# Optimization experiments

Measured on AMD Instinct MI355X. Metric: run time of the kernel, lower is better.

Reference implementation:

```python
import jax, jax.numpy as jnp
import numpy as np

ALPHA = 0.05      # SSGConv alpha
K_HOPS = 2        # SSGConv K
K_EIG = 16        # Laplacian PE eigenvectors
LN_EPS = 1e-5     # nn.LayerNorm default eps


def setup_inputs() -> dict:
    key = jax.random.key(0)
    ks = jax.random.split(key, 8)
    B, N, T, D = 16, 19, 1024, 64
    return {
        "features": jax.random.normal(ks[0], (B, N, T, D), jnp.float32),
        "adjacency": jax.random.uniform(ks[1], (B, T, N, N), jnp.float32),
        # edge_transform: nn.Linear(1,1)
        "edge_w": jax.random.normal(ks[2], (), jnp.float32) * 0.5,
        "edge_b": jnp.zeros((), jnp.float32),
        # SSGConv internal linear layers (out = h @ W.T + b)
        "gnn0_W": jax.random.normal(ks[3], (D, D + K_EIG), jnp.float32) / jnp.sqrt(jnp.float32(D + K_EIG)),
        "gnn0_b": jnp.zeros((D,), jnp.float32),
        "gnn1_W": jax.random.normal(ks[4], (D, D), jnp.float32) / jnp.sqrt(jnp.float32(D)),
        "gnn1_b": jnp.zeros((D,), jnp.float32),
        "ln0_g": jnp.ones((D,), jnp.float32), "ln0_b": jnp.zeros((D,), jnp.float32),
        "ln1_g": jnp.ones((D,), jnp.float32), "ln1_b": jnp.zeros((D,), jnp.float32),
    }


def _layernorm(x, g, b):
    mu = x.mean(-1, keepdims=True)
    var = ((x - mu) ** 2).mean(-1, keepdims=True)
    return (x - mu) * jax.lax.rsqrt(var + LN_EPS) * g + b


def _gcn_norm_dense(adj, edge_w, edge_b):
    """Edge transform + softplus on existing edges, then PyG gcn_norm.

    adj: (G, N, N). Existing edges are adj>0; their weights are
    softplus(w*a + b). Nodes without a self-loop get one with weight 1
    (add_remaining_self_loops). deg is the scatter over target (column) index.
    """
    G, N, _ = adj.shape
    mask = (adj > 0).astype(adj.dtype)
    w = jax.nn.softplus(adj * edge_w + edge_b) * mask
    eye = jnp.eye(N, dtype=adj.dtype)
    diag_mask = jnp.diagonal(mask, axis1=-2, axis2=-1)  # (G, N)
    w = w + (1.0 - diag_mask)[:, :, None] * eye          # remaining self-loops
    deg = w.sum(axis=-2)                                 # (G, N) column sums (target deg)
    dis = jnp.where(deg > 0, jax.lax.rsqrt(jnp.maximum(deg, 1e-30)), 0.0)
    # norm(i->j) = dis[i] * w[i,j] * dis[j]
    return dis[:, :, None] * w * dis[:, None, :]


def _dynamic_pe(adj):
    """Batched Laplacian eigenvector PE, faithful to _compute_dynamic_pe_vectorized."""
    G, N, _ = adj.shape
    a32 = adj.astype(jnp.float32)
    deg = jnp.maximum(a32.sum(-1), 1e-6)                 # row-sum degrees, clamped
    dis = jax.lax.rsqrt(deg)
    a_norm = dis[:, :, None] * a32 * dis[:, None, :]
    eye = jnp.eye(N, dtype=jnp.float32)
    lap = eye - a_norm + 1e-5 * eye                      # regularized Laplacian
    _, vecs = jnp.linalg.eigh(lap)                       # ascending eigenvalues
    pe = vecs[..., :K_EIG]                               # (G, N, K)
    signs = jnp.sign(pe.sum(-2, keepdims=True))
    signs = jnp.where(signs == 0, 1.0, signs)
    pe = jnp.nan_to_num(pe * signs, nan=0.0, posinf=1.0, neginf=-1.0)
    return pe


def _ssgconv(a_norm, x, W, b):
    """SSGConv: h = alpha*x + sum_{k=1..K} (1-alpha)/K * P^k x; out = h @ W.T + b.
    Propagation: out[j] = sum_i norm(i->j) x[i]  (source->target flow)."""
    h = ALPHA * x
    xk = x
    for _ in range(K_HOPS):
        xk = jnp.einsum('gij,gid->gjd', a_norm, xk)
        h = h + ((1.0 - ALPHA) / K_HOPS) * xk
    return jnp.einsum('gnd,od->gno', h, W) + b


def reference(features, adjacency, edge_w, edge_b,
              gnn0_W, gnn0_b, gnn1_W, gnn1_b,
              ln0_g, ln0_b, ln1_g, ln1_b):
    B, N, T, D = features.shape
    x = features.transpose(0, 2, 1, 3).reshape(B * T, N, D)   # (G, N, D)
    adj = adjacency.reshape(B * T, N, N)
    a_norm = _gcn_norm_dense(adj, edge_w, edge_b)
    pe = _dynamic_pe(adj).astype(features.dtype)
    # layer 0: input = [x, pe], no residual
    h = _ssgconv(a_norm, jnp.concatenate([x, pe], axis=-1), gnn0_W, gnn0_b)
    h = _layernorm(h, ln0_g, ln0_b)                            # dropout is identity (eval)
    # layer 1: input = previous output, residual add
    h = _ssgconv(a_norm, h, gnn1_W, gnn1_b) + h
    h = _layernorm(h, ln1_g, ln1_b)
    return h.reshape(B, T, N, D).transpose(0, 2, 1, 3)         # (B, N, T, D)
```

## Files before the change

kernel.cpp:

```cpp
#include <hip/hip_runtime.h>
#include <math.h>

#define Nn 19
#define Dd 64
#define KE 16
#define DIN 80
#define Tt 1024
#define Bb 16
#define Gg (Bb*Tt)
#define ALPHAc 0.05f
#define HOPW 0.475f
#define LNEPS 1e-5f

#define AN_STRIDE 384
#define PE_STRIDE 304
#define WS_NEED ((size_t)Gg * (AN_STRIDE + PE_STRIDE) * 4)

__device__ __forceinline__ float softplusf(float x){
  return (x > 0.f) ? (x + log1pf(expf(-x))) : log1pf(expf(x));
}

__device__ __forceinline__ float wsum(float v){
  #pragma unroll
  for (int o = 32; o > 0; o >>= 1) v += __shfl_xor(v, o, 64);
  return v;
}

__device__ __forceinline__ float rlanef(float v, int l){
  return __int_as_float(__builtin_amdgcn_readlane(__float_as_int(v), l));
}

__device__ __forceinline__ void wsync(){
  __asm__ volatile("" ::: "memory");
  __builtin_amdgcn_wave_barrier();
  __asm__ volatile("" ::: "memory");
}

#define ARENA_BYTES 4832
__global__ __launch_bounds__(256)
void eig_kernel(const float* __restrict__ adj,
                const float* __restrict__ ew_p, const float* __restrict__ eb_p,
                float* __restrict__ anW, float* __restrict__ peW)
{
  const int wid  = threadIdx.x >> 6;
  const int lane = threadIdx.x & 63;
  const int g    = blockIdx.x * 4 + wid;

  __shared__ __align__(16) char arenaAll[4 * ARENA_BYTES];
  char* arena = arenaAll + wid * ARENA_BYTES;
  float*  Af  = (float*) (arena);
  float*  Vf  = (float*) (arena + 1600);
  float*  adjS= (float*) (arena + 1600);
  float*  peB = (float*) (arena + 3136);
  float*  wS  = (float*) (arena + 3136);
  float*  rsS = (float*) (arena + 4592);
  float*  csS = (float*) (arena + 4672);
  float2* cs2 = (float2*)(arena + 4752);

  const float ew = ew_p[0], eb = eb_p[0];

  for (int idx = lane; idx < Nn*Nn; idx += 64)
    adjS[idx] = adj[(size_t)g*(Nn*Nn) + idx];
  wsync();

  for (int idx = lane; idx < Nn*Nn; idx += 64) {
    int i = idx / Nn, j = idx - i*Nn;
    float a = adjS[idx];
    wS[idx] = (a > 0.f) ? softplusf(a*ew + eb) : ((i == j) ? 1.f : 0.f);
  }
  if (lane < Nn) {
    float rs = 0.f;
    for (int j = 0; j < Nn; ++j) rs += adjS[lane*Nn + j];
    rsS[lane] = rsqrtf(fmaxf(rs, 1e-6f));
  }
  wsync();
  if (lane < Nn) {
    float cs = 0.f;
    for (int i = 0; i < Nn; ++i) cs += wS[i*Nn + lane];
    csS[lane] = (cs > 0.f) ? rsqrtf(fmaxf(cs, 1e-30f)) : 0.f;
  }
  wsync();
  for (int idx = lane; idx < Nn*Nn; idx += 64) {
    int i = idx / Nn, j = idx - i*Nn;
    anW[(size_t)g*AN_STRIDE + j*20 + i] = csS[i]*wS[idx]*csS[j];
  }
  for (int idx = lane; idx < Nn*Nn; idx += 64) {
    int i = idx / Nn, j = idx - i*Nn;
    float anij = rsS[i]*adjS[i*Nn + j]*rsS[j];
    float anji = rsS[j]*adjS[j*Nn + i]*rsS[i];
    Af[i*21 + j] = ((i == j) ? (1.f + 1e-5f) : 0.f) - 0.5f*(anij + anji);
  }
  if (lane < Nn) { Af[lane*21 + 19] = 0.f; Af[lane*21 + 20] = 0.f; }
  wsync();
  for (int idx = lane; idx < Nn*20; idx += 64) {
    int c = idx / 20, r2 = idx - c*20;
    Vf[idx] = (r2 == c) ? 1.f : 0.f;
  }
  wsync();

  int li = 0, lj = 0;
  if (lane < 36) {
    int l = lane, row = 0, cnt = 8;
    while (l >= cnt) { l -= cnt; ++row; --cnt; }
    li = row; lj = row + 1 + l;
  } else if (lane < 45) {
    li = lj = lane - 36;
  } else if (lane < 54) {
    li = lane - 45; lj = 0;
  }
  int ai = li + 1, bi = 18 - li;
  int aj = lj + 1, bj = 18 - lj;
  const int jv = lane % 9;
  int av = jv + 1, bv = 18 - jv;
  const int mrow = (lane / 9) * 4;
  int rr = 0;

  for (int sweep = 0; sweep < 14; ++sweep) {
    if (sweep) {
      float off = 0.f;
      for (int idx = lane; idx < Nn*21; idx += 64) {
        int i2 = idx / 21, j2 = idx - i2*21;
        float v = Af[idx];
        off += (j2 > i2 && j2 < Nn) ? v*v : 0.f;
      }
      off = wsum(off);
      if (off < 5e-10f) break;
    }

    for (int r = 0; r < Nn; ++r) {
      bool active = false;
      if (lane < 9) {
        int a = rr + 1 + lane;  if (a >= 19) a -= 19;
        int b = rr + 18 - lane; if (b >= 19) b -= 19;
        int p = min(a, b), q = max(a, b);
        float apq = Af[p*21 + q];
        float c = 1.f, s = 0.f;
        if (fabsf(apq) > 1e-12f) {
          float app = Af[p*22], aqq = Af[q*22];
          float tau = (aqq - app) / (2.f*apq);
          float tt  = sqrtf(1.f + tau*tau);
          float tv  = (tau >= 0.f) ? 1.f/(tau + tt) : 1.f/(tau - tt);
          c = rsqrtf(1.f + tv*tv);
          s = tv*c;
          active = true;
        }
        cs2[lane] = make_float2(c, s);
      }
      int anyact = __any(active);
      wsync();

      if (anyact) {
        if (lane < 45) {
          int pi = min(ai, bi), qi = max(ai, bi);
          int pj = min(aj, bj), qj = max(aj, bj);
          float2 csi = cs2[li], csj = cs2[lj];
          int a00 = (pi < pj) ? pi*21 + pj : pj*21 + pi;
          int a01 = (pi < qj) ? pi*21 + qj : qj*21 + pi;
          int a10 = (qi < pj) ? qi*21 + pj : pj*21 + qi;
          int a11 = (qi < qj) ? qi*21 + qj : qj*21 + qi;
          float App = Af[a00], Apq = Af[a01], Aqp = Af[a10], Aqq = Af[a11];
          float B0 = csj.x*App - csj.y*Apq;
          float B1 = csj.y*App + csj.x*Apq;
          float B2 = csj.x*Aqp - csj.y*Aqq;
          float B3 = csj.y*Aqp + csj.x*Aqq;
          Af[a00] = csi.x*B0 - csi.y*B2;
          Af[a01] = csi.x*B1 - csi.y*B3;
          Af[a10] = csi.y*B0 + csi.x*B2;
          Af[a11] = csi.y*B1 + csi.x*B3;
        } else if (lane < 54) {
          int p = min(ai, bi), q = max(ai, bi);
          float2 cs = cs2[li];
          int b = rr;
          int e0 = (b < p) ? b*21 + p : p*21 + b;
          int e1 = (b < q) ? b*21 + q : q*21 + b;
          float ep = Af[e0], eq = Af[e1];
          Af[e0] = cs.x*ep - cs.y*eq;
          Af[e1] = cs.y*ep + cs.x*eq;
        }
        if (lane < 45) {
          int pv = min(av, bv), qv = max(av, bv);
          float2 cs = cs2[jv];
          float4 vp = *(const float4*)(Vf + pv*20 + mrow);
          float4 vq = *(const float4*)(Vf + qv*20 + mrow);
          float4 np, nq;
          np.x = cs.x*vp.x - cs.y*vq.x;  nq.x = cs.y*vp.x + cs.x*vq.x;
          np.y = cs.x*vp.y - cs.y*vq.y;  nq.y = cs.y*vp.y + cs.x*vq.y;
          np.z = cs.x*vp.z - cs.y*vq.z;  nq.z = cs.y*vp.z + cs.x*vq.z;
          np.w = cs.x*vp.w - cs.y*vq.w;  nq.w = cs.y*vp.w + cs.x*vq.w;
          *(float4*)(Vf + pv*20 + mrow) = np;
          *(float4*)(Vf + qv*20 + mrow) = nq;
        }
        wsync();
      }

      ++ai; if (ai >= 19) ai = 0;
      ++bi; if (bi >= 19) bi = 0;
      ++aj; if (aj >= 19) aj = 0;
      ++bj; if (bj >= 19) bj = 0;
      ++av; if (av >= 19) av = 0;
      ++bv; if (bv >= 19) bv = 0;
      ++rr; if (rr >= 19) rr = 0;
    }
  }

  if (lane < Nn) {
    float lam = Af[lane*22];
    int rk = 0;
    for (int j = 0; j < Nn; ++j) {
      float lj2 = Af[j*22];
      rk += (lj2 < lam) || (lj2 == lam && j < lane);
    }
    if (rk < KE) {
      float sacc = 0.f;
      for (int n = 0; n < Nn; ++n) sacc += Vf[lane*20 + n];
      float sgn = (sacc < 0.f) ? -1.f : 1.f;
      for (int n = 0; n < Nn; ++n) peB[n*KE + rk] = Vf[lane*20 + n]*sgn;
    }
  }
  wsync();
  for (int idx = lane; idx < Nn*KE; idx += 64)
    peW[(size_t)g*PE_STRIDE + idx] = peB[idx];
}

__global__ __launch_bounds__(64)
void gnn_kernel(const float* __restrict__ feat,
                const float* __restrict__ anW, const float* __restrict__ peW,
                const float* __restrict__ W0, const float* __restrict__ b0,
                const float* __restrict__ W1, const float* __restrict__ b1,
                const float* __restrict__ g0, const float* __restrict__ be0,
                const float* __restrict__ g1, const float* __restrict__ be1,
                float* __restrict__ out)
{
  const int g = blockIdx.x, lane = threadIdx.x;
  const int b = g >> 10, t = g & (Tt - 1);

  const float* an = anW + (size_t)g*AN_STRIDE;

  float xa[Nn], xb[Nn];
  const float* fb = feat + (((size_t)b*Nn)*Tt + t)*Dd + lane;
  #pragma unroll
  for (int n = 0; n < Nn; ++n) xa[n] = fb[(size_t)n*Tt*Dd];
  #pragma unroll
  for (int n = 0; n < Nn; ++n)
    xb[n] = (lane < KE) ? peW[(size_t)g*PE_STRIDE + n*KE + lane] : 0.f;

  float x1a[Nn], x1b[Nn];
  for (int j = 0; j < Nn; ++j) {
    float aa = 0.f, ab = 0.f;
    #pragma unroll
    for (int i = 0; i < Nn; ++i) {
      float av = an[j*20 + i];
      aa = fmaf(av, xa[i], aa);
      ab = fmaf(av, xb[i], ab);
    }
    x1a[j] = aa; x1b[j] = ab;
  }
  float h0a[Nn], h0b[Nn];
  #pragma unroll
  for (int n = 0; n < Nn; ++n) {
    h0a[n] = ALPHAc*xa[n] + HOPW*x1a[n];
    h0b[n] = ALPHAc*xb[n] + HOPW*x1b[n];
  }
  for (int j = 0; j < Nn; ++j) {
    float aa = 0.f, ab = 0.f;
    #pragma unroll
    for (int i = 0; i < Nn; ++i) {
      float av = an[j*20 + i];
      aa = fmaf(av, x1a[i], aa);
      ab = fmaf(av, x1b[i], ab);
    }
    h0a[j] += HOPW*aa;
    h0b[j] += HOPW*ab;
  }

  float acc[Nn];
  #pragma unroll
  for (int n = 0; n < Nn; ++n) acc[n] = 0.f;
  {
    const float* w0p = W0 + lane*DIN;
    #pragma unroll
    for (int kb = 0; kb < 64; kb += 16) {
      float w[16];
      #pragma unroll
      for (int q4 = 0; q4 < 4; ++q4)
        *(float4*)&w[4*q4] = *(const float4*)(w0p + kb + 4*q4);
      #pragma unroll
      for (int kk = 0; kk < 16; ++kk) {
        int k = kb + kk;
        #pragma unroll
        for (int n = 0; n < Nn; ++n)
          acc[n] = fmaf(rlanef(h0a[n], k), w[kk], acc[n]);
      }
    }
    float w[16];
    #pragma unroll
    for (int q4 = 0; q4 < 4; ++q4)
      *(float4*)&w[4*q4] = *(const float4*)(w0p + 64 + 4*q4);
    #pragma unroll
    for (int kk = 0; kk < 16; ++kk) {
      #pragma unroll
      for (int n = 0; n < Nn; ++n)
        acc[n] = fmaf(rlanef(h0b[n], kk), w[kk], acc[n]);
    }
  }
  float yv[Nn];
  {
    float bias = b0[lane], gam = g0[lane], bet = be0[lane];
    #pragma unroll
    for (int n = 0; n < Nn; ++n) {
      float v  = acc[n] + bias;
      float mu = wsum(v)*(1.f/64.f);
      float d  = v - mu;
      float var = wsum(d*d)*(1.f/64.f);
      yv[n] = d*rsqrtf(var + LNEPS)*gam + bet;
    }
  }

  float x1c[Nn];
  for (int j = 0; j < Nn; ++j) {
    float aa = 0.f;
    #pragma unroll
    for (int i = 0; i < Nn; ++i)
      aa = fmaf(an[j*20 + i], yv[i], aa);
    x1c[j] = aa;
  }
  float h1[Nn];
  #pragma unroll
  for (int n = 0; n < Nn; ++n) h1[n] = ALPHAc*yv[n] + HOPW*x1c[n];
  for (int j = 0; j < Nn; ++j) {
    float aa = 0.f;
    #pragma unroll
    for (int i = 0; i < Nn; ++i)
      aa = fmaf(an[j*20 + i], x1c[i], aa);
    h1[j] += HOPW*aa;
  }

  float acc1[Nn];
  #pragma unroll
  for (int n = 0; n < Nn; ++n) acc1[n] = 0.f;
  {
    const float* w1p = W1 + lane*Dd;
    #pragma unroll
    for (int kb = 0; kb < 64; kb += 16) {
      float w[16];
      #pragma unroll
      for (int q4 = 0; q4 < 4; ++q4)
        *(float4*)&w[4*q4] = *(const float4*)(w1p + kb + 4*q4);
      #pragma unroll
      for (int kk = 0; kk < 16; ++kk) {
        int k = kb + kk;
        #pragma unroll
        for (int n = 0; n < Nn; ++n)
          acc1[n] = fmaf(rlanef(h1[n], k), w[kk], acc1[n]);
      }
    }
  }
  {
    float bias = b1[lane], gam = g1[lane], bet = be1[lane];
    float* ob = out + (((size_t)b*Nn)*Tt + t)*Dd + lane;
    #pragma unroll
    for (int n = 0; n < Nn; ++n) {
      float v  = acc1[n] + bias + yv[n];
      float mu = wsum(v)*(1.f/64.f);
      float d  = v - mu;
      float var = wsum(d*d)*(1.f/64.f);
      ob[(size_t)n*Tt*Dd] = d*rsqrtf(var + LNEPS)*gam + bet;
    }
  }
}

__global__ __launch_bounds__(64)
void gcm_mono(
  const float* __restrict__ feat,
  const float* __restrict__ adj,
  const float* __restrict__ ew_p, const float* __restrict__ eb_p,
  const float* __restrict__ W0, const float* __restrict__ b0,
  const float* __restrict__ W1, const float* __restrict__ b1,
  const float* __restrict__ g0, const float* __restrict__ be0,
  const float* __restrict__ g1, const float* __restrict__ be1,
  float* __restrict__ out)
{
  const int g    = blockIdx.x;
  const int lane = threadIdx.x;
  const int b    = g >> 10;
  const int t    = g & (Tt - 1);

  __shared__ float  anS[Nn*Nn];
  __shared__ float  peS[Nn*KE];
  __shared__ double evS[Nn];
  __shared__ float  rsS[Nn];
  __shared__ float  csS[Nn];
  __shared__ __align__(16) char arena[6080];
  double* Ad   = (double*)(arena);
  float*  Vf   = (float*)(arena + 3040);
  float*  adjS = (float*)(arena + 4560);
  float*  hb   = (float*)(arena);

  float xr[Nn];
  const float* fb = feat + (((size_t)b*Nn)*Tt + t)*Dd + lane;
  #pragma unroll
  for (int n = 0; n < Nn; ++n) xr[n] = fb[(size_t)n*Tt*Dd];

  const float ew = ew_p[0], eb = eb_p[0];

  for (int idx = lane; idx < Nn*Nn; idx += 64)
    adjS[idx] = adj[(size_t)g*(Nn*Nn) + idx];
  __syncthreads();

  if (lane < Nn) {
    float rs = 0.f;
    for (int j = 0; j < Nn; ++j) rs += adjS[lane*Nn + j];
    rsS[lane] = rsqrtf(fmaxf(rs, 1e-6f));
  }
  for (int idx = lane; idx < Nn*Nn; idx += 64) {
    int i = idx / Nn, j = idx - i*Nn;
    float a = adjS[idx];
    bool m = a > 0.f;
    float wv = m ? softplusf(a*ew + eb) : ((i == j) ? 1.f : 0.f);
    anS[idx] = wv;
  }
  __syncthreads();
  if (lane < Nn) {
    float cs = 0.f;
    for (int i = 0; i < Nn; ++i) cs += anS[i*Nn + lane];
    csS[lane] = (cs > 0.f) ? rsqrtf(fmaxf(cs, 1e-30f)) : 0.f;
  }
  __syncthreads();
  for (int idx = lane; idx < Nn*Nn; idx += 64) {
    int i = idx / Nn, j = idx - i*Nn;
    anS[idx] = csS[i]*anS[idx]*csS[j];
    float anij = rsS[i]*adjS[i*Nn + j]*rsS[j];
    float anji = rsS[j]*adjS[j*Nn + i]*rsS[i];
    double m = ((i == j) ? (1.0 + 1e-5) : 0.0) - 0.5*((double)anij + (double)anji);
    Ad[i*20 + j] = m;
    Vf[i*20 + j] = (i == j) ? 1.f : 0.f;
  }
  __syncthreads();

  for (int sweep = 0; sweep < 30; ++sweep) {
    double off = 0.0;
    for (int idx = lane; idx < Nn*Nn; idx += 64) {
      int i = idx / Nn, j = idx - i*Nn;
      if (i < j) { double v = Ad[i*20 + j]; off += v*v; }
    }
    #pragma unroll
    for (int o = 32; o > 0; o >>= 1) off += __shfl_xor(off, o, 64);
    if (off < 1e-22) break;
    for (int p = 0; p < Nn - 1; ++p) {
      for (int q = p + 1; q < Nn; ++q) {
        double apq = Ad[p*20 + q];
        if (fabs(apq) > 1e-15) {
          double app = Ad[p*20 + p], aqq = Ad[q*20 + q];
          double tau = (aqq - app) / (2.0*apq);
          double tt  = sqrt(1.0 + tau*tau);
          double tv  = (tau >= 0.0) ? 1.0/(tau + tt) : 1.0/(tau - tt);
          double c   = 1.0/sqrt(1.0 + tv*tv);
          double s   = tv*c;
          double akp = 0.0, akq = 0.0; float vkp = 0.f, vkq = 0.f;
          if (lane < Nn) {
            akp = Ad[lane*20 + p]; akq = Ad[lane*20 + q];
            vkp = Vf[lane*20 + p]; vkq = Vf[lane*20 + q];
          }
          __syncthreads();
          if (lane < Nn) {
            double nkp = c*akp - s*akq;
            double nkq = s*akp + c*akq;
            if (lane == p) {
              nkp = c*c*app - 2.0*c*s*apq + s*s*aqq;
              nkq = 0.0;
            } else if (lane == q) {
              nkp = 0.0;
              nkq = s*s*app + 2.0*c*s*apq + c*c*aqq;
            }
            Ad[lane*20 + p] = nkp; Ad[p*20 + lane] = nkp;
            Ad[lane*20 + q] = nkq; Ad[q*20 + lane] = nkq;
            float fc = (float)c, fs = (float)s;
            Vf[lane*20 + p] = fc*vkp - fs*vkq;
            Vf[lane*20 + q] = fs*vkp + fc*vkq;
          }
          __syncthreads();
        }
      }
    }
  }

  if (lane < Nn) evS[lane] = Ad[lane*20 + lane];
  __syncthreads();
  if (lane < Nn) {
    double lam = evS[lane];
    int r = 0;
    for (int j = 0; j < Nn; ++j) {
      double lj = evS[j];
      r += (lj < lam) || (lj == lam && j < lane);
    }
    if (r < KE) {
      float sacc = 0.f;
      for (int n = 0; n < Nn; ++n) sacc += Vf[n*20 + lane];
      float sgn = (sacc < 0.f) ? -1.f : 1.f;
      for (int n = 0; n < Nn; ++n) peS[n*KE + r] = Vf[n*20 + lane]*sgn;
    }
  }
  __syncthreads();

  {
    float x1[Nn], x2[Nn];
    for (int j = 0; j < Nn; ++j) {
      float a2 = 0.f;
      #pragma unroll
      for (int i = 0; i < Nn; ++i) a2 += anS[i*Nn + j]*xr[i];
      x1[j] = a2;
    }
    for (int j = 0; j < Nn; ++j) {
      float a2 = 0.f;
      #pragma unroll
      for (int i = 0; i < Nn; ++i) a2 += anS[i*Nn + j]*x1[i];
      x2[j] = a2;
    }
    #pragma unroll
    for (int n = 0; n < Nn; ++n)
      hb[n*DIN + lane] = ALPHAc*xr[n] + HOPW*(x1[n] + x2[n]);
  }
  if (lane < KE) {
    float xc[Nn], x1[Nn], x2[Nn];
    #pragma unroll
    for (int n = 0; n < Nn; ++n) xc[n] = peS[n*KE + lane];
    for (int j = 0; j < Nn; ++j) {
      float a2 = 0.f;
      #pragma unroll
      for (int i = 0; i < Nn; ++i) a2 += anS[i*Nn + j]*xc[i];
      x1[j] = a2;
    }
    for (int j = 0; j < Nn; ++j) {
      float a2 = 0.f;
      #pragma unroll
      for (int i = 0; i < Nn; ++i) a2 += anS[i*Nn + j]*x1[i];
      x2[j] = a2;
    }
    #pragma unroll
    for (int n = 0; n < Nn; ++n)
      hb[n*DIN + Dd + lane] = ALPHAc*xc[n] + HOPW*(x1[n] + x2[n]);
  }
  __syncthreads();

  float acc[Nn];
  #pragma unroll
  for (int n = 0; n < Nn; ++n) acc[n] = 0.f;
  {
    const float* w0r = W0 + lane*DIN;
    #pragma unroll 8
    for (int k = 0; k < DIN; ++k) {
      float wv = w0r[k];
      #pragma unroll
      for (int n = 0; n < Nn; ++n) acc[n] += hb[n*DIN + k]*wv;
    }
  }
  float yv[Nn];
  {
    float bias = b0[lane], gam = g0[lane], bet = be0[lane];
    #pragma unroll
    for (int n = 0; n < Nn; ++n) {
      float v  = acc[n] + bias;
      float mu = wsum(v)*(1.f/64.f);
      float d  = v - mu;
      float var = wsum(d*d)*(1.f/64.f);
      yv[n] = d*rsqrtf(var + LNEPS)*gam + bet;
    }
  }

  {
    float x1[Nn], x2[Nn];
    for (int j = 0; j < Nn; ++j) {
      float a2 = 0.f;
      #pragma unroll
      for (int i = 0; i < Nn; ++i) a2 += anS[i*Nn + j]*yv[i];
      x1[j] = a2;
    }
    for (int j = 0; j < Nn; ++j) {
      float a2 = 0.f;
      #pragma unroll
      for (int i = 0; i < Nn; ++i) a2 += anS[i*Nn + j]*x1[i];
      x2[j] = a2;
    }
    __syncthreads();
    #pragma unroll
    for (int n = 0; n < Nn; ++n)
      hb[n*Dd + lane] = ALPHAc*yv[n] + HOPW*(x1[n] + x2[n]);
    __syncthreads();
  }

  float acc1[Nn];
  #pragma unroll
  for (int n = 0; n < Nn; ++n) acc1[n] = 0.f;
  {
    const float* w1r = W1 + lane*Dd;
    #pragma unroll 8
    for (int k = 0; k < Dd; ++k) {
      float wv = w1r[k];
      #pragma unroll
      for (int n = 0; n < Nn; ++n) acc1[n] += hb[n*Dd + k]*wv;
    }
  }
  {
    float bias = b1[lane], gam = g1[lane], bet = be1[lane];
    float* ob = out + (((size_t)b*Nn)*Tt + t)*Dd + lane;
    #pragma unroll
    for (int n = 0; n < Nn; ++n) {
      float v  = acc1[n] + bias + yv[n];
      float mu = wsum(v)*(1.f/64.f);
      float d  = v - mu;
      float var = wsum(d*d)*(1.f/64.f);
      ob[(size_t)n*Tt*Dd] = d*rsqrtf(var + LNEPS)*gam + bet;
    }
  }
}

extern "C" void kernel_launch(void* const* d_in, const int* in_sizes, int n_in,
                              void* d_out, int out_size, void* d_ws, size_t ws_size,
                              hipStream_t stream) {
  (void)in_sizes; (void)n_in; (void)out_size;
  const float* feat = (const float*)d_in[0];
  const float* adj  = (const float*)d_in[1];
  const float* ew   = (const float*)d_in[2];
  const float* eb   = (const float*)d_in[3];
  const float* W0   = (const float*)d_in[4];
  const float* b0   = (const float*)d_in[5];
  const float* W1   = (const float*)d_in[6];
  const float* b1   = (const float*)d_in[7];
  const float* g0   = (const float*)d_in[8];
  const float* be0  = (const float*)d_in[9];
  const float* g1   = (const float*)d_in[10];
  const float* be1  = (const float*)d_in[11];
  float* out = (float*)d_out;

  if (ws_size >= WS_NEED) {
    float* anW = (float*)d_ws;
    float* peW = anW + (size_t)Gg*AN_STRIDE;
    hipLaunchKernelGGL(eig_kernel, dim3(Gg/4), dim3(256), 0, stream,
                       adj, ew, eb, anW, peW);
    hipLaunchKernelGGL(gnn_kernel, dim3(Gg), dim3(64), 0, stream,
                       feat, anW, peW, W0, b0, W1, b1, g0, be0, g1, be1, out);
  } else {
    hipLaunchKernelGGL(gcm_mono, dim3(Gg), dim3(64), 0, stream,
                       feat, adj, ew, eb, W0, b0, W1, b1, g0, be0, g1, be1, out);
  }
}
```

Before: 790.3 us.

## Keep Jacobi eigenvector matrix in registers with readlane-broadcast rotations

Moves the eigenvector accumulator V of the cyclic Jacobi solver from LDS into a per-lane register array of 19 floats. Each lane owns one row, rotation coefficients are broadcast with readlane, and the register array is rotated at the end of each round so the rotation pairs stay at fixed indices. Rotation parameters are now computed redundantly on all lanes with hardware rcp/sqrt/rsq intrinsics instead of IEEE divide and sqrt, and the LDS arena is reshuffled. This is meant to remove LDS traffic and float4 load/store work from the inner rotation step. It adds register pressure, slightly lower-precision intrinsics, and extra register moves for the cyclic shift.

```diff
diff --git a/kernel.cpp b/kernel.cpp
--- a/kernel.cpp
+++ b/kernel.cpp
@@ -36,7 +36,7 @@
   __asm__ volatile("" ::: "memory");
 }
 
-#define ARENA_BYTES 4832
+#define ARENA_BYTES 4944
 __global__ __launch_bounds__(256)
 void eig_kernel(const float* __restrict__ adj,
                 const float* __restrict__ ew_p, const float* __restrict__ eb_p,
@@ -49,13 +49,13 @@
   __shared__ __align__(16) char arenaAll[4 * ARENA_BYTES];
   char* arena = arenaAll + wid * ARENA_BYTES;
   float*  Af  = (float*) (arena);
-  float*  Vf  = (float*) (arena + 1600);
+  float*  Vst = (float*) (arena + 1600);
   float*  adjS= (float*) (arena + 1600);
-  float*  peB = (float*) (arena + 3136);
-  float*  wS  = (float*) (arena + 3136);
-  float*  rsS = (float*) (arena + 4592);
-  float*  csS = (float*) (arena + 4672);
-  float2* cs2 = (float2*)(arena + 4752);
+  float*  peB = (float*) (arena + 3200);
+  float*  wS  = (float*) (arena + 3200);
+  float*  rsS = (float*) (arena + 4704);
+  float*  csS = (float*) (arena + 4784);
+  float2* cs2 = (float2*)(arena + 4864);
 
   const float ew = ew_p[0], eb = eb_p[0];
 
@@ -91,11 +91,6 @@
     Af[i*21 + j] = ((i == j) ? (1.f + 1e-5f) : 0.f) - 0.5f*(anij + anji);
   }
   if (lane < Nn) { Af[lane*21 + 19] = 0.f; Af[lane*21 + 20] = 0.f; }
-  wsync();
-  for (int idx = lane; idx < Nn*20; idx += 64) {
-    int c = idx / 20, r2 = idx - c*20;
-    Vf[idx] = (r2 == c) ? 1.f : 0.f;
-  }
   wsync();
 
   int li = 0, lj = 0;
@@ -108,49 +103,58 @@
   } else if (lane < 54) {
     li = lane - 45; lj = 0;
   }
-  int ai = li + 1, bi = 18 - li;
-  int aj = lj + 1, bj = 18 - lj;
-  const int jv = lane % 9;
-  int av = jv + 1, bv = 18 - jv;
-  const int mrow = (lane / 9) * 4;
-  int rr = 0;
+  const int la9 = lane % 9;
+
+  float v[Nn];
+  #pragma unroll
+  for (int c = 0; c < Nn; ++c) v[c] = (lane == c) ? 1.f : 0.f;
 
   for (int sweep = 0; sweep < 14; ++sweep) {
     if (sweep) {
       float off = 0.f;
       for (int idx = lane; idx < Nn*21; idx += 64) {
         int i2 = idx / 21, j2 = idx - i2*21;
-        float v = Af[idx];
-        off += (j2 > i2 && j2 < Nn) ? v*v : 0.f;
+        float vv = Af[idx];
+        off += (j2 > i2 && j2 < Nn) ? vv*vv : 0.f;
       }
       off = wsum(off);
       if (off < 5e-10f) break;
     }
 
+    #pragma unroll 1
     for (int r = 0; r < Nn; ++r) {
-      bool active = false;
-      if (lane < 9) {
-        int a = rr + 1 + lane;  if (a >= 19) a -= 19;
-        int b = rr + 18 - lane; if (b >= 19) b -= 19;
-        int p = min(a, b), q = max(a, b);
-        float apq = Af[p*21 + q];
-        float c = 1.f, s = 0.f;
-        if (fabsf(apq) > 1e-12f) {
-          float app = Af[p*22], aqq = Af[q*22];
-          float tau = (aqq - app) / (2.f*apq);
-          float tt  = sqrtf(1.f + tau*tau);
-          float tv  = (tau >= 0.f) ? 1.f/(tau + tt) : 1.f/(tau - tt);
-          c = rsqrtf(1.f + tv*tv);
-          s = tv*c;
-          active = true;
+      int aA = r + 1 + la9;  if (aA >= Nn) aA -= Nn;
+      int bA = r + 18 - la9; if (bA >= Nn) bA -= Nn;
+      int pA = min(aA, bA), qA = max(aA, bA);
+      float apq = Af[pA*21 + qA];
+      float app = Af[pA*22], aqq = Af[qA*22];
+      bool act = fabsf(apq) > 1e-12f;
+      float tau = (aqq - app) * 0.5f * __builtin_amdgcn_rcpf(apq);
+      float tt  = __builtin_amdgcn_sqrtf(fmaf(tau, tau, 1.f));
+      float tv  = __builtin_amdgcn_rcpf(tau + ((tau >= 0.f) ? tt : -tt));
+      float cN  = __builtin_amdgcn_rsqf(fmaf(tv, tv, 1.f));
+      float sN  = tv * cN;
+      float cc    = act ? cN : 1.f;
+      float ss    = act ? sN : 0.f;
+      float sSlot = (aA < bA) ? ss : -ss;
+      if (lane < 9) cs2[lane] = make_float2(cc, ss);
+      int anyact = __any(act && (lane < 9));
+      wsync();
+
+      if (anyact) {
+        #pragma unroll
+        for (int t2 = 0; t2 < 9; ++t2) {
+          float ct = rlanef(cc, t2);
+          float st = rlanef(sSlot, t2);
+          float vp = v[1 + t2], vq = v[18 - t2];
+          v[1 + t2]  = fmaf(ct, vp, -st*vq);
+          v[18 - t2] = fmaf(st, vp,  ct*vq);
         }
-        cs2[lane] = make_float2(c, s);
-      }
-      int anyact = __any(active);
-      wsync();
-
-      if (anyact) {
         if (lane < 45) {
+          int ai = li + 1 + r;  if (ai >= Nn) ai -= Nn;
+          int bi = 18 - li + r; if (bi >= Nn) bi -= Nn;
+          int aj = lj + 1 + r;  if (aj >= Nn) aj -= Nn;
+          int bj = 18 - lj + r; if (bj >= Nn) bj -= Nn;
           int pi = min(ai, bi), qi = max(ai, bi);
           int pj = min(aj, bj), qj = max(aj, bj);
           float2 csi = cs2[li], csj = cs2[lj];
@@ -168,40 +172,32 @@
           Af[a10] = csi.y*B0 + csi.x*B2;
           Af[a11] = csi.y*B1 + csi.x*B3;
         } else if (lane < 54) {
+          int ai = li + 1 + r;  if (ai >= Nn) ai -= Nn;
+          int bi = 18 - li + r; if (bi >= Nn) bi -= Nn;
           int p = min(ai, bi), q = max(ai, bi);
           float2 cs = cs2[li];
-          int b = rr;
-          int e0 = (b < p) ? b*21 + p : p*21 + b;
-          int e1 = (b < q) ? b*21 + q : q*21 + b;
+          int e0 = (r < p) ? r*21 + p : p*21 + r;
+          int e1 = (r < q) ? r*21 + q : q*21 + r;
           float ep = Af[e0], eq = Af[e1];
           Af[e0] = cs.x*ep - cs.y*eq;
           Af[e1] = cs.y*ep + cs.x*eq;
         }
-        if (lane < 45) {
-          int pv = min(av, bv), qv = max(av, bv);
-          float2 cs = cs2[jv];
-          float4 vp = *(const float4*)(Vf + pv*20 + mrow);
-          float4 vq = *(const float4*)(Vf + qv*20 + mrow);
-          float4 np, nq;
-          np.x = cs.x*vp.x - cs.y*vq.x;  nq.x = cs.y*vp.x + cs.x*vq.x;
-          np.y = cs.x*vp.y - cs.y*vq.y;  nq.y = cs.y*vp.y + cs.x*vq.y;
-          np.z = cs.x*vp.z - cs.y*vq.z;  nq.z = cs.y*vp.z + cs.x*vq.z;
-          np.w = cs.x*vp.w - cs.y*vq.w;  nq.w = cs.y*vp.w + cs.x*vq.w;
-          *(float4*)(Vf + pv*20 + mrow) = np;
-          *(float4*)(Vf + qv*20 + mrow) = nq;
-        }
         wsync();
       }
 
-      ++ai; if (ai >= 19) ai = 0;
-      ++bi; if (bi >= 19) bi = 0;
-      ++aj; if (aj >= 19) aj = 0;
-      ++bj; if (bj >= 19) bj = 0;
-      ++av; if (av >= 19) av = 0;
-      ++bv; if (bv >= 19) bv = 0;
-      ++rr; if (rr >= 19) rr = 0;
-    }
-  }
+      {
+        float t0 = v[0];
+        #pragma unroll
+        for (int c = 0; c < Nn - 1; ++c) v[c] = v[c + 1];
+        v[Nn - 1] = t0;
+      }
+    }
+  }
+
+  #pragma unroll
+  for (int c = 0; c < Nn; ++c)
+    if (lane < Nn) Vst[c*20 + lane] = v[c];
+  wsync();
 
   if (lane < Nn) {
     float lam = Af[lane*22];
@@ -212,9 +208,9 @@
     }
     if (rk < KE) {
       float sacc = 0.f;
-      for (int n = 0; n < Nn; ++n) sacc += Vf[lane*20 + n];
+      for (int n = 0; n < Nn; ++n) sacc += Vst[lane*20 + n];
       float sgn = (sacc < 0.f) ? -1.f : 1.f;
-      for (int n = 0; n < Nn; ++n) peB[n*KE + rk] = Vf[lane*20 + n]*sgn;
+      for (int n = 0; n < Nn; ++n) peB[n*KE + rk] = Vst[lane*20 + n]*sgn;
     }
   }
   wsync();
```

Measured after the change: 882.0 us. 11.6% more time.
